# Performance work log

Measured on AMD Instinct MI355X. Metric: run time of the kernel, lower is better.

Reference implementation:

```python
import jax, jax.numpy as jnp
import numpy as np

EMB_LEN = 1024
HEAD_SIZE = 64

def setup_inputs() -> dict:
    key = jax.random.key(0)
    k1, k2, k3, k4 = jax.random.split(key, 4)
    input_emb = jax.random.normal(k1, (8, 4096, EMB_LEN), dtype=jnp.float32)
    # nn.Linear weights are [out, in]; applied as x @ W.T
    Wq = jax.random.normal(k2, (HEAD_SIZE, EMB_LEN), dtype=jnp.float32) * (EMB_LEN ** -0.5)
    Wk = jax.random.normal(k3, (HEAD_SIZE, EMB_LEN), dtype=jnp.float32) * (EMB_LEN ** -0.5)
    Wv = jax.random.normal(k4, (HEAD_SIZE, EMB_LEN), dtype=jnp.float32) * (EMB_LEN ** -0.5)
    return {"input_emb": input_emb, "Wq": Wq, "Wk": Wk, "Wv": Wv}

def reference(input_emb, Wq, Wk, Wv):
    B, S, E = input_emb.shape
    scale = jnp.asarray(HEAD_SIZE, input_emb.dtype) ** -0.5
    q = jnp.einsum('bse,he->bsh', input_emb, Wq)  # [B,S,H]
    k = jnp.einsum('bse,he->bsh', input_emb, Wk)
    v = jnp.einsum('bse,he->bsh', input_emb, Wv)
    scores = jnp.einsum('bqh,bkh->bqk', q, k) * scale  # [B,S,S]
    causal = jnp.tril(jnp.ones((S, S), dtype=bool))
    scores = jnp.where(causal, scores, -jnp.inf)
    attn = jax.nn.softmax(scores, axis=-1)
    return jnp.einsum('bqk,bkh->bqh', attn, v)
```

## Files before the change

### kernel.cpp

```cpp
#include <hip/hip_runtime.h>
#include <hip/hip_bf16.h>

#define EMB 1024
#define HS 64
#define SEQ 4096

using bf16x8 = __attribute__((ext_vector_type(8))) __bf16;
using f32x4  = __attribute__((ext_vector_type(4))) float;

__device__ __forceinline__ ushort f2b(float f) {
    unsigned x = __float_as_uint(f);
    return (ushort)((x + 0x7fffu + ((x >> 16) & 1u)) >> 16);
}

__global__ void cvt_w(const float* __restrict__ wq, const float* __restrict__ wk,
                      const float* __restrict__ wv, ushort* __restrict__ wcat) {
    int i = blockIdx.x * 256 + threadIdx.x;
    const int n = HS * EMB;
    if (i >= 3 * n) return;
    float f;
    if (i < n)          f = wq[i];
    else if (i < 2 * n) f = wk[i - n];
    else                f = wv[i - 2 * n];
    wcat[i] = f2b(f);
}

__global__ __launch_bounds__(1024) void qkv_proj(
        const float* __restrict__ x, const ushort* __restrict__ wcat,
        ushort* __restrict__ qo, ushort* __restrict__ ko, ushort* __restrict__ vo) {
    __shared__ ushort Xs[64][72];
    __shared__ ushort Ws[192][72];
    const int t = threadIdx.x;
    const int lane = t & 63, wid = t >> 6;
    const int g = lane >> 4, c = lane & 15;
    const int strip = wid >> 2, colq = wid & 3;
    const int row0 = blockIdx.x * 64;

    f32x4 acc[3];
#pragma unroll
    for (int i = 0; i < 3; ++i) acc[i] = f32x4{0.f, 0.f, 0.f, 0.f};

    for (int kc = 0; kc < EMB; kc += 64) {
        __syncthreads();
        {
            int e = t * 4, r = e >> 6, cc = e & 63;
            float4 v = *reinterpret_cast<const float4*>(&x[(row0 + r) * EMB + kc + cc]);
            ushort4 u;
            u.x = f2b(v.x); u.y = f2b(v.y); u.z = f2b(v.z); u.w = f2b(v.w);
            *reinterpret_cast<ushort4*>(&Xs[r][cc]) = u;
        }
#pragma unroll
        for (int i = 0; i < 3; ++i) {
            int e = (i * 1024 + t) * 4, r = e >> 6, cc = e & 63;
            *reinterpret_cast<ushort4*>(&Ws[r][cc]) =
                *reinterpret_cast<const ushort4*>(&wcat[r * EMB + kc + cc]);
        }
        __syncthreads();
#pragma unroll
        for (int kk = 0; kk < 2; ++kk) {
            bf16x8 a = *reinterpret_cast<const bf16x8*>(&Xs[strip * 16 + c][kk * 32 + 8 * g]);
#pragma unroll
            for (int nt = 0; nt < 3; ++nt) {
                bf16x8 b = *reinterpret_cast<const bf16x8*>(
                    &Ws[(colq * 3 + nt) * 16 + c][kk * 32 + 8 * g]);
                acc[nt] = __builtin_amdgcn_mfma_f32_16x16x32_bf16(a, b, acc[nt], 0, 0, 0);
            }
        }
    }

    const float qs = 0.125f * 1.44269504f;
#pragma unroll
    for (int nt = 0; nt < 3; ++nt) {
        int col = (colq * 3 + nt) * 16 + c;
        int rowb = row0 + strip * 16 + 4 * g;
        if (col < 64) {
#pragma unroll
            for (int r = 0; r < 4; ++r)
                qo[(rowb + r) * 64 + col] = f2b(acc[nt][r] * qs);
        } else if (col < 128) {
#pragma unroll
            for (int r = 0; r < 4; ++r)
                ko[(rowb + r) * 64 + (col - 64)] = f2b(acc[nt][r]);
        } else {
            int b = rowb >> 12, s0 = rowb & 4095;
            ushort4 pv;
            pv.x = f2b(acc[nt][0]); pv.y = f2b(acc[nt][1]);
            pv.z = f2b(acc[nt][2]); pv.w = f2b(acc[nt][3]);
            *reinterpret_cast<ushort4*>(&vo[(b * 64 + (col - 128)) * SEQ + s0]) = pv;
        }
    }
}

__global__ __launch_bounds__(256) void attn(
        const ushort* __restrict__ q, const ushort* __restrict__ k,
        const ushort* __restrict__ vt, float* __restrict__ out) {
    __shared__ __align__(16) char smem[40960];

    const int t = threadIdx.x;
    const int lane = t & 63, w = t >> 6;
    const int g = lane >> 4, c = lane & 15;
    const int sp = w & 1, pp = w >> 1;

    const int bid = blockIdx.x;
    const int batch = bid & 7;
    const int qt = 63 - (bid >> 3);
    const int q0b = qt * 64;
    const int npairs = qt + 1;

    const char* kbp = (const char*)(k + (size_t)batch * SEQ * 64);
    const char* vbp = (const char*)(vt + (size_t)batch * 64 * SEQ);
    const ushort* qb = q + (size_t)batch * SEQ * 64;

    auto stage_pair = [&](int cpair, char* base) {
#pragma unroll
        for (int n = 0; n < 4; ++n) {
            int idx = w * 4 + n;
            int cpar = idx >> 3, rest = idx & 7, isV = rest >> 2, f = rest & 3;
            int kv0 = (cpair * 2 + cpar) * 32;
            const char* src;
            if (!isV)
                src = kbp + (size_t)(kv0 + (f >> 1) * 16 + c) * 128 + (f & 1) * 64 + 16 * g;
            else
                src = vbp + (size_t)(f * 16 + c) * (SEQ * 2) + kv0 * 2 + 16 * g;
            char* dst = base + cpar * 8192 + isV * 4096 + f * 1024;
            __builtin_amdgcn_global_load_lds(
                (const __attribute__((address_space(1))) void*)src,
                (__attribute__((address_space(3))) void*)dst, 16, 0, 0);
        }
    };

    bf16x8 qa[2][2];
#pragma unroll
    for (int ss = 0; ss < 2; ++ss)
#pragma unroll
        for (int kk = 0; kk < 2; ++kk)
            qa[ss][kk] = *reinterpret_cast<const bf16x8*>(
                &qb[(q0b + sp * 32 + ss * 16 + c) * 64 + kk * 32 + 8 * g]);

    f32x4 accO[2][4];
#pragma unroll
    for (int ss = 0; ss < 2; ++ss)
#pragma unroll
        for (int nt = 0; nt < 4; ++nt) accO[ss][nt] = f32x4{0.f, 0.f, 0.f, 0.f};
    float lsum[2][4] = {{0.f, 0.f, 0.f, 0.f}, {0.f, 0.f, 0.f, 0.f}};

    stage_pair(0, smem);

    const int pbase = 32768 + w * 2048 + (((c >> 3) * 16 + 4 * g) * 16) + (c & 7) * 2;

    for (int cpair = 0; cpair < npairs; ++cpair) {
        asm volatile("s_waitcnt vmcnt(0)" ::: "memory");
        __builtin_amdgcn_s_barrier();
        __builtin_amdgcn_sched_barrier(0);

        if (cpair + 1 < npairs)
            stage_pair(cpair + 1, smem + ((cpair + 1) & 1) * 16384);

        const char* tb = smem + (cpair & 1) * 16384 + pp * 8192;

        f32x4 sA[2][2];
#pragma unroll
        for (int ss = 0; ss < 2; ++ss)
#pragma unroll
            for (int kt = 0; kt < 2; ++kt) sA[ss][kt] = f32x4{0.f, 0.f, 0.f, 0.f};
        __builtin_amdgcn_s_setprio(1);
#pragma unroll
        for (int kk = 0; kk < 2; ++kk)
#pragma unroll
            for (int kt = 0; kt < 2; ++kt) {
                bf16x8 kf = *reinterpret_cast<const bf16x8*>(tb + (kt * 2 + kk) * 1024 + lane * 16);
                sA[0][kt] = __builtin_amdgcn_mfma_f32_16x16x32_bf16(qa[0][kk], kf, sA[0][kt], 0, 0, 0);
                sA[1][kt] = __builtin_amdgcn_mfma_f32_16x16x32_bf16(qa[1][kk], kf, sA[1][kt], 0, 0, 0);
            }
        __builtin_amdgcn_s_setprio(0);

        if (cpair == npairs - 1) {
#pragma unroll
            for (int ss = 0; ss < 2; ++ss)
#pragma unroll
                for (int kt = 0; kt < 2; ++kt) {
                    int kvl = pp * 32 + kt * 16 + c;
#pragma unroll
                    for (int r = 0; r < 4; ++r) {
                        int ql = sp * 32 + ss * 16 + 4 * g + r;
                        if (kvl > ql) sA[ss][kt][r] = -INFINITY;
                    }
                }
        }

#pragma unroll
        for (int ss = 0; ss < 2; ++ss)
#pragma unroll
            for (int kt = 0; kt < 2; ++kt)
#pragma unroll
                for (int r = 0; r < 4; ++r) {
                    float p = __builtin_amdgcn_exp2f(sA[ss][kt][r]);
                    lsum[ss][r] += p;
                    *(ushort*)(smem + pbase + ss * 1024 + kt * 512 + r * 16) = f2b(p);
                }

        bf16x8 pa0 = *reinterpret_cast<const bf16x8*>(smem + 32768 + w * 2048 + lane * 16);
        bf16x8 pa1 = *reinterpret_cast<const bf16x8*>(smem + 32768 + w * 2048 + 1024 + lane * 16);

        __builtin_amdgcn_s_setprio(1);
#pragma unroll
        for (int nt = 0; nt < 4; ++nt) {
            bf16x8 vf = *reinterpret_cast<const bf16x8*>(tb + 4096 + nt * 1024 + lane * 16);
            accO[0][nt] = __builtin_amdgcn_mfma_f32_16x16x32_bf16(pa0, vf, accO[0][nt], 0, 0, 0);
            accO[1][nt] = __builtin_amdgcn_mfma_f32_16x16x32_bf16(pa1, vf, accO[1][nt], 0, 0, 0);
        }
        __builtin_amdgcn_s_setprio(0);
    }

#pragma unroll
    for (int off = 1; off < 16; off <<= 1)
#pragma unroll
        for (int ss = 0; ss < 2; ++ss)
#pragma unroll
            for (int r = 0; r < 4; ++r)
                lsum[ss][r] += __shfl_xor(lsum[ss][r], off, 64);

    __syncthreads();
    if (pp == 1) {
#pragma unroll
        for (int ss = 0; ss < 2; ++ss)
#pragma unroll
            for (int nt = 0; nt < 4; ++nt)
#pragma unroll
                for (int r = 0; r < 4; ++r)
                    *(float*)(smem + sp * 8192 + (ss * 16 + 4 * g + r) * 256 + (nt * 16 + c) * 4) =
                        accO[ss][nt][r];
        if (c == 0)
#pragma unroll
            for (int ss = 0; ss < 2; ++ss)
#pragma unroll
                for (int r = 0; r < 4; ++r)
                    *(float*)(smem + 16384 + sp * 128 + (ss * 16 + 4 * g + r) * 4) = lsum[ss][r];
    }
    __syncthreads();
    if (pp == 0) {
        float* ob = out + (size_t)batch * SEQ * 64;
#pragma unroll
        for (int ss = 0; ss < 2; ++ss)
#pragma unroll
            for (int nt = 0; nt < 4; ++nt)
#pragma unroll
                for (int r = 0; r < 4; ++r) {
                    float a2 = *(float*)(smem + sp * 8192 + (ss * 16 + 4 * g + r) * 256 + (nt * 16 + c) * 4);
                    float l2 = *(float*)(smem + 16384 + sp * 128 + (ss * 16 + 4 * g + r) * 4);
                    ob[(q0b + sp * 32 + ss * 16 + 4 * g + r) * 64 + nt * 16 + c] =
                        (accO[ss][nt][r] + a2) / (lsum[ss][r] + l2);
                }
    }
}

extern "C" void kernel_launch(void* const* d_in, const int* in_sizes, int n_in,
                              void* d_out, int out_size, void* d_ws, size_t ws_size,
                              hipStream_t stream) {
    const float* x  = (const float*)d_in[0];
    const float* wq = (const float*)d_in[1];
    const float* wk = (const float*)d_in[2];
    const float* wv = (const float*)d_in[3];
    float* out = (float*)d_out;

    char* ws = (char*)d_ws;
    ushort* wcat = (ushort*)ws;
    ushort* qo   = (ushort*)(ws + 393216);
    ushort* ko   = (ushort*)(ws + 393216 + 4194304);
    ushort* vo   = (ushort*)(ws + 393216 + 2 * 4194304);

    hipLaunchKernelGGL(cvt_w, dim3(768), dim3(256), 0, stream, wq, wk, wv, wcat);
    hipLaunchKernelGGL(qkv_proj, dim3(512), dim3(1024), 0, stream, x, wcat, qo, ko, vo);
    hipLaunchKernelGGL(attn, dim3(512), dim3(256), 0, stream, qo, ko, vo, out);
}
```

Before: 96.74 us.

## Split-KV attention across waves with register-prefetched K/V and smaller query tiles

```diff
diff --git a/kernel.cpp b/kernel.cpp
--- a/kernel.cpp
+++ b/kernel.cpp
@@ -94,40 +94,22 @@
 __global__ __launch_bounds__(256) void attn(
         const ushort* __restrict__ q, const ushort* __restrict__ k,
         const ushort* __restrict__ vt, float* __restrict__ out) {
-    __shared__ __align__(16) char smem[40960];
+    __shared__ __align__(16) char smem[33280];
 
     const int t = threadIdx.x;
     const int lane = t & 63, w = t >> 6;
     const int g = lane >> 4, c = lane & 15;
-    const int sp = w & 1, pp = w >> 1;
 
     const int bid = blockIdx.x;
     const int batch = bid & 7;
-    const int qt = 63 - (bid >> 3);
-    const int q0b = qt * 64;
-    const int npairs = qt + 1;
-
-    const char* kbp = (const char*)(k + (size_t)batch * SEQ * 64);
-    const char* vbp = (const char*)(vt + (size_t)batch * 64 * SEQ);
-    const ushort* qb = q + (size_t)batch * SEQ * 64;
-
-    auto stage_pair = [&](int cpair, char* base) {
-#pragma unroll
-        for (int n = 0; n < 4; ++n) {
-            int idx = w * 4 + n;
-            int cpar = idx >> 3, rest = idx & 7, isV = rest >> 2, f = rest & 3;
-            int kv0 = (cpair * 2 + cpar) * 32;
-            const char* src;
-            if (!isV)
-                src = kbp + (size_t)(kv0 + (f >> 1) * 16 + c) * 128 + (f & 1) * 64 + 16 * g;
-            else
-                src = vbp + (size_t)(f * 16 + c) * (SEQ * 2) + kv0 * 2 + 16 * g;
-            char* dst = base + cpar * 8192 + isV * 4096 + f * 1024;
-            __builtin_amdgcn_global_load_lds(
-                (const __attribute__((address_space(1))) void*)src,
-                (__attribute__((address_space(3))) void*)dst, 16, 0, 0);
-        }
-    };
+    const int qt = 127 - (bid >> 3);
+    const int q0 = qt * 32;
+    const int nch = qt + 1;
+    const int c0 = (w * nch) >> 2, c1 = ((w + 1) * nch) >> 2;
+
+    const ushort* qb = q  + (size_t)batch * SEQ * 64;
+    const ushort* kb = k  + (size_t)batch * SEQ * 64;
+    const ushort* vb = vt + (size_t)batch * 64 * SEQ;
 
     bf16x8 qa[2][2];
 #pragma unroll
@@ -135,7 +117,7 @@
 #pragma unroll
         for (int kk = 0; kk < 2; ++kk)
             qa[ss][kk] = *reinterpret_cast<const bf16x8*>(
-                &qb[(q0b + sp * 32 + ss * 16 + c) * 64 + kk * 32 + 8 * g]);
+                &qb[(q0 + ss * 16 + c) * 64 + kk * 32 + 8 * g]);
 
     f32x4 accO[2][4];
 #pragma unroll
@@ -144,20 +126,24 @@
         for (int nt = 0; nt < 4; ++nt) accO[ss][nt] = f32x4{0.f, 0.f, 0.f, 0.f};
     float lsum[2][4] = {{0.f, 0.f, 0.f, 0.f}, {0.f, 0.f, 0.f, 0.f}};
 
-    stage_pair(0, smem);
-
-    const int pbase = 32768 + w * 2048 + (((c >> 3) * 16 + 4 * g) * 16) + (c & 7) * 2;
-
-    for (int cpair = 0; cpair < npairs; ++cpair) {
-        asm volatile("s_waitcnt vmcnt(0)" ::: "memory");
-        __builtin_amdgcn_s_barrier();
-        __builtin_amdgcn_sched_barrier(0);
-
-        if (cpair + 1 < npairs)
-            stage_pair(cpair + 1, smem + ((cpair + 1) & 1) * 16384);
-
-        const char* tb = smem + (cpair & 1) * 16384 + pp * 8192;
-
+    char* const pslice = smem + w * 2048;
+    const int pwr = (c >> 3) * 256 + g * 64 + (c & 7) * 2;
+
+    auto loadkv = [&](bf16x8 (&kf)[2][2], bf16x8 (&vf)[4], int ch) {
+        const int kv0 = ch * 32;
+#pragma unroll
+        for (int kt = 0; kt < 2; ++kt)
+#pragma unroll
+            for (int kk = 0; kk < 2; ++kk)
+                kf[kt][kk] = *reinterpret_cast<const bf16x8*>(
+                    &kb[(kv0 + kt * 16 + c) * 64 + kk * 32 + 8 * g]);
+#pragma unroll
+        for (int nt = 0; nt < 4; ++nt)
+            vf[nt] = *reinterpret_cast<const bf16x8*>(
+                &vb[(nt * 16 + c) * SEQ + kv0 + 8 * g]);
+    };
+
+    auto compute = [&](bf16x8 (&kf)[2][2], bf16x8 (&vf)[4], int ch) {
         f32x4 sA[2][2];
 #pragma unroll
         for (int ss = 0; ss < 2; ++ss)
@@ -168,24 +154,19 @@
         for (int kk = 0; kk < 2; ++kk)
 #pragma unroll
             for (int kt = 0; kt < 2; ++kt) {
-                bf16x8 kf = *reinterpret_cast<const bf16x8*>(tb + (kt * 2 + kk) * 1024 + lane * 16);
-                sA[0][kt] = __builtin_amdgcn_mfma_f32_16x16x32_bf16(qa[0][kk], kf, sA[0][kt], 0, 0, 0);
-                sA[1][kt] = __builtin_amdgcn_mfma_f32_16x16x32_bf16(qa[1][kk], kf, sA[1][kt], 0, 0, 0);
+                sA[0][kt] = __builtin_amdgcn_mfma_f32_16x16x32_bf16(qa[0][kk], kf[kt][kk], sA[0][kt], 0, 0, 0);
+                sA[1][kt] = __builtin_amdgcn_mfma_f32_16x16x32_bf16(qa[1][kk], kf[kt][kk], sA[1][kt], 0, 0, 0);
             }
         __builtin_amdgcn_s_setprio(0);
 
-        if (cpair == npairs - 1) {
+        if (ch == nch - 1) {
 #pragma unroll
             for (int ss = 0; ss < 2; ++ss)
 #pragma unroll
-                for (int kt = 0; kt < 2; ++kt) {
-                    int kvl = pp * 32 + kt * 16 + c;
-#pragma unroll
-                    for (int r = 0; r < 4; ++r) {
-                        int ql = sp * 32 + ss * 16 + 4 * g + r;
-                        if (kvl > ql) sA[ss][kt][r] = -INFINITY;
-                    }
-                }
+                for (int kt = 0; kt < 2; ++kt)
+#pragma unroll
+                    for (int r = 0; r < 4; ++r)
+                        if (kt * 16 + c > ss * 16 + 4 * g + r) sA[ss][kt][r] = -INFINITY;
         }
 
 #pragma unroll
@@ -196,20 +177,33 @@
                 for (int r = 0; r < 4; ++r) {
                     float p = __builtin_amdgcn_exp2f(sA[ss][kt][r]);
                     lsum[ss][r] += p;
-                    *(ushort*)(smem + pbase + ss * 1024 + kt * 512 + r * 16) = f2b(p);
+                    *(ushort*)(pslice + ss * 1024 + kt * 512 + r * 16 + pwr) = f2b(p);
                 }
 
-        bf16x8 pa0 = *reinterpret_cast<const bf16x8*>(smem + 32768 + w * 2048 + lane * 16);
-        bf16x8 pa1 = *reinterpret_cast<const bf16x8*>(smem + 32768 + w * 2048 + 1024 + lane * 16);
+        bf16x8 pa0 = *reinterpret_cast<const bf16x8*>(pslice + lane * 16);
+        bf16x8 pa1 = *reinterpret_cast<const bf16x8*>(pslice + 1024 + lane * 16);
 
         __builtin_amdgcn_s_setprio(1);
 #pragma unroll
         for (int nt = 0; nt < 4; ++nt) {
-            bf16x8 vf = *reinterpret_cast<const bf16x8*>(tb + 4096 + nt * 1024 + lane * 16);
-            accO[0][nt] = __builtin_amdgcn_mfma_f32_16x16x32_bf16(pa0, vf, accO[0][nt], 0, 0, 0);
-            accO[1][nt] = __builtin_amdgcn_mfma_f32_16x16x32_bf16(pa1, vf, accO[1][nt], 0, 0, 0);
+            accO[0][nt] = __builtin_amdgcn_mfma_f32_16x16x32_bf16(pa0, vf[nt], accO[0][nt], 0, 0, 0);
+            accO[1][nt] = __builtin_amdgcn_mfma_f32_16x16x32_bf16(pa1, vf[nt], accO[1][nt], 0, 0, 0);
         }
         __builtin_amdgcn_s_setprio(0);
+    };
+
+    bf16x8 kfA[2][2], vfA[4], kfB[2][2], vfB[4];
+    int ch = c0;
+    if (ch < c1) {
+        loadkv(kfA, vfA, ch);
+        while (true) {
+            loadkv(kfB, vfB, (ch + 1 < c1) ? ch + 1 : ch);
+            compute(kfA, vfA, ch);
+            if (++ch >= c1) break;
+            loadkv(kfA, vfA, (ch + 1 < c1) ? ch + 1 : ch);
+            compute(kfB, vfB, ch);
+            if (++ch >= c1) break;
+        }
     }
 
 #pragma unroll
@@ -221,36 +215,35 @@
                 lsum[ss][r] += __shfl_xor(lsum[ss][r], off, 64);
 
     __syncthreads();
-    if (pp == 1) {
-#pragma unroll
-        for (int ss = 0; ss < 2; ++ss)
-#pragma unroll
-            for (int nt = 0; nt < 4; ++nt)
-#pragma unroll
-                for (int r = 0; r < 4; ++r)
-                    *(float*)(smem + sp * 8192 + (ss * 16 + 4 * g + r) * 256 + (nt * 16 + c) * 4) =
-                        accO[ss][nt][r];
-        if (c == 0)
-#pragma unroll
-            for (int ss = 0; ss < 2; ++ss)
-#pragma unroll
-                for (int r = 0; r < 4; ++r)
-                    *(float*)(smem + 16384 + sp * 128 + (ss * 16 + 4 * g + r) * 4) = lsum[ss][r];
+#pragma unroll
+    for (int ss = 0; ss < 2; ++ss)
+#pragma unroll
+        for (int nt = 0; nt < 4; ++nt)
+#pragma unroll
+            for (int r = 0; r < 4; ++r)
+                *(float*)(smem + w * 8192 + (ss * 16 + 4 * g + r) * 256 + (nt * 16 + c) * 4) =
+                    accO[ss][nt][r];
+    if (c == 0) {
+#pragma unroll
+        for (int ss = 0; ss < 2; ++ss)
+#pragma unroll
+            for (int r = 0; r < 4; ++r)
+                *(float*)(smem + 32768 + w * 128 + (ss * 16 + 4 * g + r) * 4) = lsum[ss][r];
     }
     __syncthreads();
-    if (pp == 0) {
-        float* ob = out + (size_t)batch * SEQ * 64;
-#pragma unroll
-        for (int ss = 0; ss < 2; ++ss)
-#pragma unroll
-            for (int nt = 0; nt < 4; ++nt)
-#pragma unroll
-                for (int r = 0; r < 4; ++r) {
-                    float a2 = *(float*)(smem + sp * 8192 + (ss * 16 + 4 * g + r) * 256 + (nt * 16 + c) * 4);
-                    float l2 = *(float*)(smem + 16384 + sp * 128 + (ss * 16 + 4 * g + r) * 4);
-                    ob[(q0b + sp * 32 + ss * 16 + 4 * g + r) * 64 + nt * 16 + c] =
-                        (accO[ss][nt][r] + a2) / (lsum[ss][r] + l2);
-                }
+
+    float* ob = out + (size_t)batch * SEQ * 64;
+    const int col = t & 63, r0 = t >> 6;
+#pragma unroll
+    for (int rr = 0; rr < 8; ++rr) {
+        int row = rr * 4 + r0;
+        float s = 0.f, l = 0.f;
+#pragma unroll
+        for (int w4 = 0; w4 < 4; ++w4) {
+            s += *(float*)(smem + w4 * 8192 + row * 256 + col * 4);
+            l += *(float*)(smem + 32768 + w4 * 128 + row * 4);
+        }
+        ob[(q0 + row) * 64 + col] = s / l;
     }
 }
 
@@ -271,5 +264,5 @@
 
     hipLaunchKernelGGL(cvt_w, dim3(768), dim3(256), 0, stream, wq, wk, wv, wcat);
     hipLaunchKernelGGL(qkv_proj, dim3(512), dim3(1024), 0, stream, x, wcat, qo, ko, vo);
-    hipLaunchKernelGGL(attn, dim3(512), dim3(256), 0, stream, qo, ko, vo, out);
-}
+    hipLaunchKernelGGL(attn, dim3(1024), dim3(256), 0, stream, qo, ko, vo, out);
+}
```

New measurement: 111.9 us. +15.7%, slower.
